# Kernel optimization log

Measured on AMD Instinct MI355X. Metric: run time of the kernel, lower is better.

The kernel has to match this reference:

```python
import jax, jax.numpy as jnp
import numpy as np

D_MODEL, D_K, H = 1024, 64, 16
B, S = 2, 2048

def setup_inputs() -> dict:
    key = jax.random.key(0)
    ks = jax.random.split(key, 9)
    s_in = 1.0 / np.sqrt(D_MODEL)
    x = jax.random.normal(ks[0], (B, S, D_MODEL), dtype=jnp.float32)
    Wq = jax.random.uniform(ks[1], (H, D_MODEL, D_K), jnp.float32, -s_in, s_in)
    bq = jax.random.uniform(ks[2], (H, D_K), jnp.float32, -s_in, s_in)
    Wk = jax.random.uniform(ks[3], (H, D_MODEL, D_K), jnp.float32, -s_in, s_in)
    bk = jax.random.uniform(ks[4], (H, D_K), jnp.float32, -s_in, s_in)
    Wv = jax.random.uniform(ks[5], (H, D_MODEL, D_K), jnp.float32, -s_in, s_in)
    bv = jax.random.uniform(ks[6], (H, D_K), jnp.float32, -s_in, s_in)
    Wo = jax.random.uniform(ks[7], (D_MODEL, D_MODEL), jnp.float32, -s_in, s_in)
    bo = jax.random.uniform(ks[8], (D_MODEL,), jnp.float32, -s_in, s_in)
    return {"x": x, "Wq": Wq, "bq": bq, "Wk": Wk, "bk": bk,
            "Wv": Wv, "bv": bv, "Wo": Wo, "bo": bo}

def reference(x, Wq, bq, Wk, bk, Wv, bv, Wo, bo):
    # PositionLinear = Linear + ReLU (the ReLU is part of the original math)
    Q = jax.nn.relu(jnp.einsum('bsd,hdk->bhsk', x, Wq) + bq[:, None, :])
    K = jax.nn.relu(jnp.einsum('bsd,hdk->bhsk', x, Wk) + bk[:, None, :])
    V = jax.nn.relu(jnp.einsum('bsd,hdk->bhsk', x, Wv) + bv[:, None, :])
    scale = jnp.sqrt(jnp.float32(Q.shape[-1]))
    scores = jnp.einsum('bhsk,bhtk->bhst', Q, K) / scale  # [B,H,S,S]
    attn = jax.nn.softmax(scores, axis=-1)
    ctx = jnp.einsum('bhst,bhtk->bhsk', attn, V)
    # concat heads along feature dim (head order matches torch.cat(output, 2))
    ctx = jnp.transpose(ctx, (0, 2, 1, 3)).reshape(x.shape[0], x.shape[1], -1)
    out = jax.nn.relu(ctx @ Wo + bo)
    return out
```

## Files before the change

### kernel.cpp

```cpp
#include <hip/hip_runtime.h>
#include <cstddef>

#define D_MODEL 1024
#define DK 64
#define NH 16
#define NB 2
#define SEQ 2048

typedef __attribute__((ext_vector_type(8))) short bf16x8;
typedef __attribute__((ext_vector_type(4))) float floatx4;
typedef __attribute__((ext_vector_type(2))) unsigned uintx2;

static __device__ __forceinline__ unsigned short f2bf(float f) {
    union { float f; unsigned u; } v; v.f = f;
    unsigned r = (v.u + 0x7fffu + ((v.u >> 16) & 1u)) >> 16;
    return (unsigned short)r;
}

static __device__ __forceinline__ unsigned pk2bf(float lo, float hi) {
    unsigned ua = __float_as_uint(lo) + 0x8000u;
    unsigned ub = __float_as_uint(hi) + 0x8000u;
    return __builtin_amdgcn_perm(ub, ua, 0x07060302u);
}

static __device__ __forceinline__ float swz16(float x) {
    return __int_as_float(__builtin_amdgcn_ds_swizzle(__float_as_int(x), 0x401F));
}

static __device__ __forceinline__ void gld16(const unsigned short* g, unsigned short* l) {
    __builtin_amdgcn_global_load_lds(
        (const __attribute__((address_space(1))) unsigned int*)g,
        (__attribute__((address_space(3))) unsigned int*)l, 16, 0, 0);
}

__global__ __launch_bounds__(256) void convert_x(const float* __restrict__ x,
                                                 unsigned short* __restrict__ xb)
{
    const size_t i = ((size_t)blockIdx.x * 256 + threadIdx.x) * 16;
#pragma unroll
    for (int c = 0; c < 16; c += 4) {
        float4 v = *(const float4*)&x[i + c];
        uint2 pk;
        pk.x = (unsigned)f2bf(v.x) | ((unsigned)f2bf(v.y) << 16);
        pk.y = (unsigned)f2bf(v.z) | ((unsigned)f2bf(v.w) << 16);
        *(uint2*)&xb[i + c] = pk;
    }
}

__global__ __launch_bounds__(256) void pack_w(
    const float* __restrict__ Wq, const float* __restrict__ Wk,
    const float* __restrict__ Wv, const float* __restrict__ Wo,
    unsigned short* __restrict__ Bqkv, unsigned short* __restrict__ Bo)
{
    __shared__ float T[64][65];
    const int t   = blockIdx.x;
    const int tid = threadIdx.x;
    const int rr   = tid >> 2;
    const int cseg = (tid & 3) * 16;

    const float* src;
    unsigned short* dst;
    if (t < 768) {
        const int proj = t / 256, rem = t % 256;
        const int h = rem >> 4, d0 = (rem & 15) * 64;
        const float* W = proj == 0 ? Wq : (proj == 1 ? Wk : Wv);
        src = W + ((size_t)h * 1024 + d0) * 64;
#pragma unroll
        for (int c = 0; c < 16; c += 4) {
            float4 v = *(const float4*)&src[(size_t)rr * 64 + cseg + c];
            T[rr][cseg + c + 0] = v.x; T[rr][cseg + c + 1] = v.y;
            T[rr][cseg + c + 2] = v.z; T[rr][cseg + c + 3] = v.w;
        }
        __syncthreads();
        dst = &Bqkv[((size_t)proj * 1024 + h * 64 + rr) * 1024 + d0 + cseg];
    } else {
        const int t2 = t - 768;
        const int k0 = (t2 >> 4) * 64, nb0 = (t2 & 15) * 64;
#pragma unroll
        for (int c = 0; c < 16; c += 4) {
            float4 v = *(const float4*)&Wo[(size_t)(k0 + rr) * 1024 + nb0 + cseg + c];
            T[rr][cseg + c + 0] = v.x; T[rr][cseg + c + 1] = v.y;
            T[rr][cseg + c + 2] = v.z; T[rr][cseg + c + 3] = v.w;
        }
        __syncthreads();
        dst = &Bo[(size_t)(nb0 + rr) * 1024 + k0 + cseg];
    }
    unsigned int w[8];
#pragma unroll
    for (int ii = 0; ii < 8; ii++) {
        unsigned short lo = f2bf(T[cseg + ii * 2 + 0][rr]);
        unsigned short hi = f2bf(T[cseg + ii * 2 + 1][rr]);
        w[ii] = (unsigned)lo | ((unsigned)hi << 16);
    }
    *(uint4*)(dst + 0) = make_uint4(w[0], w[1], w[2], w[3]);
    *(uint4*)(dst + 8) = make_uint4(w[4], w[5], w[6], w[7]);
}

__global__ __launch_bounds__(256) void gemm_qkv(
    const unsigned short* __restrict__ Abf,
    const unsigned short* __restrict__ Bp,
    const float* __restrict__ bq, const float* __restrict__ bk,
    const float* __restrict__ bv,
    unsigned short* __restrict__ Qo, unsigned short* __restrict__ Ko,
    unsigned short* __restrict__ Vo)
{
    __shared__ __align__(16) unsigned short As[128 * 32];
    __shared__ __align__(16) unsigned short Bs[128 * 32];

    const int tid  = threadIdx.x;
    const int wv   = tid >> 6, lane = tid & 63;
    const int m0   = blockIdx.x * 128;
    const int n0   = blockIdx.y * 128;
    const int lq   = lane & 15, g = lane >> 4;
    const int wm   = (wv >> 1) * 64;
    const int wn   = (wv & 1) * 64;
    const int srow = lane >> 2;
    const int sseg = (lane & 3) * 8;

    floatx4 acc[4][4];
#pragma unroll
    for (int i = 0; i < 4; i++)
#pragma unroll
        for (int j = 0; j < 4; j++) acc[i][j] = (floatx4){0.f, 0.f, 0.f, 0.f};

    for (int k0 = 0; k0 < 1024; k0 += 32) {
#pragma unroll
        for (int r = 0; r < 2; r++) {
            const int chunk = wv * 2 + r;
            const int row   = chunk * 16 + srow;
            gld16(&Abf[(size_t)(m0 + row) * 1024 + k0 + sseg], &As[chunk * 512]);
            gld16(&Bp [(size_t)(n0 + row) * 1024 + k0 + sseg], &Bs[chunk * 512]);
        }
        __syncthreads();
        bf16x8 af[4], bfv[4];
#pragma unroll
        for (int i = 0; i < 4; i++)
            af[i] = *(const bf16x8*)&As[(wm + i * 16 + lq) * 32 + g * 8];
#pragma unroll
        for (int j = 0; j < 4; j++)
            bfv[j] = *(const bf16x8*)&Bs[(wn + j * 16 + lq) * 32 + g * 8];
#pragma unroll
        for (int i = 0; i < 4; i++)
#pragma unroll
            for (int j = 0; j < 4; j++)
                acc[i][j] = __builtin_amdgcn_mfma_f32_16x16x32_bf16(af[i], bfv[j], acc[i][j], 0, 0, 0);
        __syncthreads();
    }

    const int proj = n0 >> 10;
    const float* bias = proj == 0 ? bq : (proj == 1 ? bk : bv);
    unsigned short* OutQK = proj == 0 ? Qo : Ko;

#pragma unroll
    for (int j = 0; j < 4; j++) {
        const int n  = n0 + wn + j * 16 + lq;
        const int nn = n & 1023;
        const int h  = nn >> 6, dk = nn & 63;
        const float bb = bias[nn];
#pragma unroll
        for (int i = 0; i < 4; i++) {
            const int mbase = m0 + wm + i * 16 + g * 4;
            const int b_ = mbase >> 11;
            const int s_ = mbase & (SEQ - 1);
            const int bh = b_ * NH + h;
            if (proj < 2) {
                const size_t fb = (((size_t)bh * 128 + (s_ >> 4)) * 2 + (dk >> 5)) * 512
                                + (size_t)((((dk & 31) >> 3) * 16) + (s_ & 15)) * 8 + (dk & 7);
#pragma unroll
                for (int r = 0; r < 4; r++)
                    OutQK[fb + (size_t)r * 8] = f2bf(fmaxf(acc[i][j][r] + bb, 0.f));
            } else {
                const size_t fb = ((((size_t)bh * 32 + (s_ >> 6)) * 4 + (dk >> 4)) * 2
                                   + ((s_ >> 5) & 1)) * 512
                                + (size_t)((((s_ & 31) >> 3) * 16) + (dk & 15)) * 8 + (s_ & 7);
                uint2 pk;
                pk.x = (unsigned)f2bf(fmaxf(acc[i][j][0] + bb, 0.f))
                     | ((unsigned)f2bf(fmaxf(acc[i][j][1] + bb, 0.f)) << 16);
                pk.y = (unsigned)f2bf(fmaxf(acc[i][j][2] + bb, 0.f))
                     | ((unsigned)f2bf(fmaxf(acc[i][j][3] + bb, 0.f)) << 16);
                *(uint2*)&Vo[fb] = pk;
            }
        }
    }
}

__global__ __launch_bounds__(512, 4) void attn_kernel(
    const unsigned short* __restrict__ Qf,
    const unsigned short* __restrict__ Kf,
    const unsigned short* __restrict__ Vf,
    unsigned short* __restrict__ ctxb)
{
    __shared__ __align__(16) unsigned short KVs[2][16384];
    __shared__ float Lx[4][2][64];

    const int blk = blockIdx.x;
    const int xcd = blk & 7;
    const int j_  = blk >> 3;
    const int bh  = xcd * 4 + (j_ & 3);
    const int qt  = j_ >> 2;

    const int tid  = threadIdx.x;
    const int wv   = tid >> 6;
    const int lane = tid & 63;
    const int lq   = lane & 15;
    const int g    = lane >> 4;
    const int qq   = wv >> 1;
    const int kh   = wv & 1;

    const int q0 = qt * 128 + qq * 32;

    bf16x8 qa[2], qb[2];
    const size_t qfB = ((size_t)bh * 128 + (q0 >> 4)) * 1024 + (size_t)lane * 8;
#pragma unroll
    for (int t = 0; t < 2; t++) {
        qa[t] = *(const bf16x8*)&Qf[qfB + (size_t)t * 1024];
        qb[t] = *(const bf16x8*)&Qf[qfB + (size_t)t * 1024 + 512];
    }

    const float C  = 0.18033688011112042f;
    const float MC = 2.8853900817779267f;

    const unsigned short* KtB = &Kf[(size_t)bh * 131072];
    const unsigned short* VtB = &Vf[(size_t)bh * 131072];

    float l[2] = {0.f, 0.f};
    floatx4 acc[2][4];
#pragma unroll
    for (int t = 0; t < 2; t++)
#pragma unroll
        for (int n = 0; n < 4; n++) acc[t][n] = (floatx4){0.f, 0.f, 0.f, 0.f};

#pragma unroll
    for (int r = 0; r < 2; r++) {
        const int c = wv * 2 + r;
        gld16(&KtB[(size_t)c * 512 + lane * 8], &KVs[0][c * 512]);
        gld16(&VtB[(size_t)c * 512 + lane * 8], &KVs[0][8192 + c * 512]);
    }
    __syncthreads();

    for (int jt = 0; jt < SEQ / 128; jt++) {
        const int buf = jt & 1;

        const int jn = (jt + 1) & (SEQ / 128 - 1);
        const unsigned short* ktn = &KtB[(size_t)jn * 8192];
        const unsigned short* vtn = &VtB[(size_t)jn * 8192];
#pragma unroll
        for (int r = 0; r < 2; r++) {
            const int c = wv * 2 + r;
            gld16(&ktn[(size_t)c * 512 + lane * 8], &KVs[buf ^ 1][c * 512]);
            gld16(&vtn[(size_t)c * 512 + lane * 8], &KVs[buf ^ 1][8192 + c * 512]);
        }

        const unsigned short* kb = &KVs[buf][0];
        const unsigned short* vb = &KVs[buf][8192];

#pragma unroll
        for (int s = 0; s < 2; s++) {
            const int kg = 4 * kh + 2 * s;
            bf16x8 a0 = *(const bf16x8*)&kb[(kg + 0) * 1024 + lane * 8];
            bf16x8 a1 = *(const bf16x8*)&kb[(kg + 0) * 1024 + 512 + lane * 8];
            bf16x8 a2 = *(const bf16x8*)&kb[(kg + 1) * 1024 + lane * 8];
            bf16x8 a3 = *(const bf16x8*)&kb[(kg + 1) * 1024 + 512 + lane * 8];
            bf16x8 vr[4];
#pragma unroll
            for (int n = 0; n < 4; n++)
                vr[n] = *(const bf16x8*)&vb[(kh * 4 + n) * 1024 + s * 512 + lane * 8];

#pragma unroll
            for (int t = 0; t < 2; t++) {
                floatx4 s0 = (floatx4){0.f, 0.f, 0.f, 0.f};
                floatx4 s1 = (floatx4){0.f, 0.f, 0.f, 0.f};
                __builtin_amdgcn_s_setprio(1);
                s0 = __builtin_amdgcn_mfma_f32_16x16x32_bf16(a0, qa[t], s0, 0, 0, 0);
                s0 = __builtin_amdgcn_mfma_f32_16x16x32_bf16(a1, qb[t], s0, 0, 0, 0);
                s1 = __builtin_amdgcn_mfma_f32_16x16x32_bf16(a2, qa[t], s1, 0, 0, 0);
                s1 = __builtin_amdgcn_mfma_f32_16x16x32_bf16(a3, qb[t], s1, 0, 0, 0);
                __builtin_amdgcn_s_setprio(0);

                float p00 = __builtin_amdgcn_exp2f(fmaf(s0[0], C, -MC));
                float p01 = __builtin_amdgcn_exp2f(fmaf(s0[1], C, -MC));
                float p02 = __builtin_amdgcn_exp2f(fmaf(s0[2], C, -MC));
                float p03 = __builtin_amdgcn_exp2f(fmaf(s0[3], C, -MC));
                l[t] += (p00 + p01) + (p02 + p03);
                unsigned d0 = pk2bf(p00, p01);
                unsigned d1 = pk2bf(p02, p03);

                float p10 = __builtin_amdgcn_exp2f(fmaf(s1[0], C, -MC));
                float p11 = __builtin_amdgcn_exp2f(fmaf(s1[1], C, -MC));
                float p12 = __builtin_amdgcn_exp2f(fmaf(s1[2], C, -MC));
                float p13 = __builtin_amdgcn_exp2f(fmaf(s1[3], C, -MC));
                l[t] += (p10 + p11) + (p12 + p13);
                unsigned d2 = pk2bf(p10, p11);
                unsigned d3 = pk2bf(p12, p13);

                uintx2 r02 = __builtin_amdgcn_permlane32_swap(d0, d2, false, false);
                uintx2 r13 = __builtin_amdgcn_permlane32_swap(d1, d3, false, false);
                uintx2 f02 = __builtin_amdgcn_permlane16_swap(r02.x, r02.y, false, false);
                uintx2 f13 = __builtin_amdgcn_permlane16_swap(r13.x, r13.y, false, false);

                union { unsigned u[4]; bf16x8 v; } pbu;
                pbu.u[0] = f02.x;
                pbu.u[1] = f13.x;
                pbu.u[2] = f02.y;
                pbu.u[3] = f13.y;

                __builtin_amdgcn_s_setprio(1);
#pragma unroll
                for (int n = 0; n < 4; n++)
                    acc[t][n] = __builtin_amdgcn_mfma_f32_16x16x32_bf16(vr[n], pbu.v, acc[t][n], 0, 0, 0);
                __builtin_amdgcn_s_setprio(0);
            }
        }

        __syncthreads();
    }

#pragma unroll
    for (int t = 0; t < 2; t++) {
        l[t] += swz16(l[t]);
        l[t] += __shfl_xor(l[t], 32, 64);
    }

    float* red = (float*)&KVs[0][0] + (size_t)qq * 2048;
    if (kh == 1) {
#pragma unroll
        for (int t = 0; t < 2; t++) {
            Lx[qq][t][lane] = l[t];
#pragma unroll
            for (int n = 0; n < 4; n++)
                *(floatx4*)&red[(t * 4 + n) * 256 + lane * 4] = acc[t][n];
        }
    }
    __syncthreads();
    if (kh == 0) {
        const int b_ = bh >> 4, h_ = bh & 15;
#pragma unroll
        for (int t = 0; t < 2; t++) {
            const float lt = l[t] + Lx[qq][t][lane];
            const float li = 1.f / lt;
#pragma unroll
            for (int n = 0; n < 4; n++) {
                floatx4 a = acc[t][n];
                floatx4 b = *(const floatx4*)&red[(t * 4 + n) * 256 + lane * 4];
                uint2 pk;
                pk.x = pk2bf((a[0] + b[0]) * li, (a[1] + b[1]) * li);
                pk.y = pk2bf((a[2] + b[2]) * li, (a[3] + b[3]) * li);
                *(uint2*)&ctxb[((size_t)(b_ * SEQ) + q0 + t * 16 + lq) * D_MODEL
                               + h_ * DK + n * 16 + g * 4] = pk;
            }
        }
    }
}

__global__ __launch_bounds__(256) void gemm_o(
    const unsigned short* __restrict__ Abf,
    const unsigned short* __restrict__ Bp,
    const float* __restrict__ bo,
    float* __restrict__ out)
{
    __shared__ __align__(16) unsigned short As[64 * 32];
    __shared__ __align__(16) unsigned short Bs[64 * 32];

    const int tid  = threadIdx.x;
    const int wv   = tid >> 6, lane = tid & 63;
    const int bid  = blockIdx.x;
    const int swz  = (bid & 7) * 128 + (bid >> 3);
    const int m0   = (swz & 63) * 64;
    const int n0   = (swz >> 6) * 64;
    const int lq   = lane & 15, g = lane >> 4;
    const int wm   = (wv >> 1) * 32;
    const int wn   = (wv & 1) * 32;
    const int srow = lane >> 2;
    const int sseg = (lane & 3) * 8;

    floatx4 acc[2][2];
#pragma unroll
    for (int i = 0; i < 2; i++)
#pragma unroll
        for (int j = 0; j < 2; j++) acc[i][j] = (floatx4){0.f, 0.f, 0.f, 0.f};

    for (int k0 = 0; k0 < 1024; k0 += 32) {
        const int row = wv * 16 + srow;
        gld16(&Abf[(size_t)(m0 + row) * 1024 + k0 + sseg], &As[wv * 512]);
        gld16(&Bp [(size_t)(n0 + row) * 1024 + k0 + sseg], &Bs[wv * 512]);
        __syncthreads();
        bf16x8 af[2], bfv[2];
#pragma unroll
        for (int i = 0; i < 2; i++)
            af[i] = *(const bf16x8*)&As[(wm + i * 16 + lq) * 32 + g * 8];
#pragma unroll
        for (int j = 0; j < 2; j++)
            bfv[j] = *(const bf16x8*)&Bs[(wn + j * 16 + lq) * 32 + g * 8];
#pragma unroll
        for (int i = 0; i < 2; i++)
#pragma unroll
            for (int j = 0; j < 2; j++)
                acc[i][j] = __builtin_amdgcn_mfma_f32_16x16x32_bf16(af[i], bfv[j], acc[i][j], 0, 0, 0);
        __syncthreads();
    }

#pragma unroll
    for (int j = 0; j < 2; j++) {
        const int n  = n0 + wn + j * 16 + lq;
        const float bb = bo[n];
#pragma unroll
        for (int i = 0; i < 2; i++) {
#pragma unroll
            for (int r = 0; r < 4; r++) {
                const int m = m0 + wm + i * 16 + g * 4 + r;
                out[(size_t)m * 1024 + n] = fmaxf(acc[i][j][r] + bb, 0.f);
            }
        }
    }
}

extern "C" void kernel_launch(void* const* d_in, const int* in_sizes, int n_in,
                              void* d_out, int out_size, void* d_ws, size_t ws_size,
                              hipStream_t stream) {
    const float* x  = (const float*)d_in[0];
    const float* Wq = (const float*)d_in[1];
    const float* bq = (const float*)d_in[2];
    const float* Wk = (const float*)d_in[3];
    const float* bk = (const float*)d_in[4];
    const float* Wv = (const float*)d_in[5];
    const float* bv = (const float*)d_in[6];
    const float* Wo = (const float*)d_in[7];
    const float* bo = (const float*)d_in[8];
    float* out = (float*)d_out;

    const size_t perE = (size_t)NB * NH * SEQ * DK;
    unsigned short* xbf  = (unsigned short*)d_ws;
    unsigned short* Bqkv = xbf  + (size_t)4096 * 1024;
    unsigned short* Bo   = Bqkv + (size_t)3072 * 1024;
    unsigned short* Qfr  = Bo   + (size_t)1024 * 1024;
    unsigned short* Kfr  = Qfr + perE;
    unsigned short* Vfr  = Kfr + perE;
    unsigned short* Cbf  = Vfr + perE;

    convert_x<<<1024, 256, 0, stream>>>(x, xbf);
    pack_w<<<1024, 256, 0, stream>>>(Wq, Wk, Wv, Wo, Bqkv, Bo);
    gemm_qkv<<<dim3(32, 24), 256, 0, stream>>>(xbf, Bqkv, bq, bk, bv, Qfr, Kfr, Vfr);
    attn_kernel<<<512, 512, 0, stream>>>(Qfr, Kfr, Vfr, Cbf);
    gemm_o<<<1024, 256, 0, stream>>>(Cbf, Bo, bo, out);
}
```

Before: 193.2 us.

## Read K/V fragments directly from global memory in attention and merge prep kernels

The attention kernel drops its double-buffered LDS staging of K/V tiles (global_load_lds plus a per-iteration barrier). Each wave now loads its K and V fragments straight from global memory, relying on cache reuse across the waves of a block. It also removes the s_setprio hints around the MFMAs and unrolls the key loop by two. The x conversion and weight packing kernels are merged into one launch to save a kernel launch. The risk is redundant global/L2 traffic, because each K/V tile is now read by several waves instead of once into shared memory.

```diff
diff --git a/kernel.cpp b/kernel.cpp
--- a/kernel.cpp
+++ b/kernel.cpp
@@ -33,28 +33,29 @@
         (__attribute__((address_space(3))) unsigned int*)l, 16, 0, 0);
 }
 
-__global__ __launch_bounds__(256) void convert_x(const float* __restrict__ x,
-                                                 unsigned short* __restrict__ xb)
-{
-    const size_t i = ((size_t)blockIdx.x * 256 + threadIdx.x) * 16;
-#pragma unroll
-    for (int c = 0; c < 16; c += 4) {
-        float4 v = *(const float4*)&x[i + c];
-        uint2 pk;
-        pk.x = (unsigned)f2bf(v.x) | ((unsigned)f2bf(v.y) << 16);
-        pk.y = (unsigned)f2bf(v.z) | ((unsigned)f2bf(v.w) << 16);
-        *(uint2*)&xb[i + c] = pk;
-    }
-}
-
-__global__ __launch_bounds__(256) void pack_w(
+__global__ __launch_bounds__(256) void prep(
+    const float* __restrict__ x, unsigned short* __restrict__ xb,
     const float* __restrict__ Wq, const float* __restrict__ Wk,
     const float* __restrict__ Wv, const float* __restrict__ Wo,
     unsigned short* __restrict__ Bqkv, unsigned short* __restrict__ Bo)
 {
     __shared__ float T[64][65];
-    const int t   = blockIdx.x;
     const int tid = threadIdx.x;
+
+    if (blockIdx.x < 1024) {
+        const size_t i = ((size_t)blockIdx.x * 256 + tid) * 16;
+#pragma unroll
+        for (int c = 0; c < 16; c += 4) {
+            float4 v = *(const float4*)&x[i + c];
+            uint2 pk;
+            pk.x = (unsigned)f2bf(v.x) | ((unsigned)f2bf(v.y) << 16);
+            pk.y = (unsigned)f2bf(v.z) | ((unsigned)f2bf(v.w) << 16);
+            *(uint2*)&xb[i + c] = pk;
+        }
+        return;
+    }
+
+    const int t   = blockIdx.x - 1024;
     const int rr   = tid >> 2;
     const int cseg = (tid & 3) * 16;
 
@@ -190,7 +191,7 @@
     const unsigned short* __restrict__ Vf,
     unsigned short* __restrict__ ctxb)
 {
-    __shared__ __align__(16) unsigned short KVs[2][16384];
+    __shared__ float red[4][2048];
     __shared__ float Lx[4][2][64];
 
     const int blk = blockIdx.x;
@@ -230,29 +231,10 @@
 #pragma unroll
         for (int n = 0; n < 4; n++) acc[t][n] = (floatx4){0.f, 0.f, 0.f, 0.f};
 
-#pragma unroll
-    for (int r = 0; r < 2; r++) {
-        const int c = wv * 2 + r;
-        gld16(&KtB[(size_t)c * 512 + lane * 8], &KVs[0][c * 512]);
-        gld16(&VtB[(size_t)c * 512 + lane * 8], &KVs[0][8192 + c * 512]);
-    }
-    __syncthreads();
-
+#pragma unroll 2
     for (int jt = 0; jt < SEQ / 128; jt++) {
-        const int buf = jt & 1;
-
-        const int jn = (jt + 1) & (SEQ / 128 - 1);
-        const unsigned short* ktn = &KtB[(size_t)jn * 8192];
-        const unsigned short* vtn = &VtB[(size_t)jn * 8192];
-#pragma unroll
-        for (int r = 0; r < 2; r++) {
-            const int c = wv * 2 + r;
-            gld16(&ktn[(size_t)c * 512 + lane * 8], &KVs[buf ^ 1][c * 512]);
-            gld16(&vtn[(size_t)c * 512 + lane * 8], &KVs[buf ^ 1][8192 + c * 512]);
-        }
-
-        const unsigned short* kb = &KVs[buf][0];
-        const unsigned short* vb = &KVs[buf][8192];
+        const unsigned short* kb = KtB + (size_t)jt * 8192;
+        const unsigned short* vb = VtB + (size_t)jt * 8192;
 
 #pragma unroll
         for (int s = 0; s < 2; s++) {
@@ -270,12 +252,10 @@
             for (int t = 0; t < 2; t++) {
                 floatx4 s0 = (floatx4){0.f, 0.f, 0.f, 0.f};
                 floatx4 s1 = (floatx4){0.f, 0.f, 0.f, 0.f};
-                __builtin_amdgcn_s_setprio(1);
                 s0 = __builtin_amdgcn_mfma_f32_16x16x32_bf16(a0, qa[t], s0, 0, 0, 0);
                 s0 = __builtin_amdgcn_mfma_f32_16x16x32_bf16(a1, qb[t], s0, 0, 0, 0);
                 s1 = __builtin_amdgcn_mfma_f32_16x16x32_bf16(a2, qa[t], s1, 0, 0, 0);
                 s1 = __builtin_amdgcn_mfma_f32_16x16x32_bf16(a3, qb[t], s1, 0, 0, 0);
-                __builtin_amdgcn_s_setprio(0);
 
                 float p00 = __builtin_amdgcn_exp2f(fmaf(s0[0], C, -MC));
                 float p01 = __builtin_amdgcn_exp2f(fmaf(s0[1], C, -MC));
@@ -304,15 +284,11 @@
                 pbu.u[2] = f02.y;
                 pbu.u[3] = f13.y;
 
-                __builtin_amdgcn_s_setprio(1);
 #pragma unroll
                 for (int n = 0; n < 4; n++)
                     acc[t][n] = __builtin_amdgcn_mfma_f32_16x16x32_bf16(vr[n], pbu.v, acc[t][n], 0, 0, 0);
-                __builtin_amdgcn_s_setprio(0);
             }
         }
-
-        __syncthreads();
     }
 
 #pragma unroll
@@ -321,14 +297,13 @@
         l[t] += __shfl_xor(l[t], 32, 64);
     }
 
-    float* red = (float*)&KVs[0][0] + (size_t)qq * 2048;
     if (kh == 1) {
 #pragma unroll
         for (int t = 0; t < 2; t++) {
             Lx[qq][t][lane] = l[t];
 #pragma unroll
             for (int n = 0; n < 4; n++)
-                *(floatx4*)&red[(t * 4 + n) * 256 + lane * 4] = acc[t][n];
+                *(floatx4*)&red[qq][(t * 4 + n) * 256 + lane * 4] = acc[t][n];
         }
     }
     __syncthreads();
@@ -341,7 +316,7 @@
 #pragma unroll
             for (int n = 0; n < 4; n++) {
                 floatx4 a = acc[t][n];
-                floatx4 b = *(const floatx4*)&red[(t * 4 + n) * 256 + lane * 4];
+                floatx4 b = *(const floatx4*)&red[qq][(t * 4 + n) * 256 + lane * 4];
                 uint2 pk;
                 pk.x = pk2bf((a[0] + b[0]) * li, (a[1] + b[1]) * li);
                 pk.y = pk2bf((a[2] + b[2]) * li, (a[3] + b[3]) * li);
@@ -437,8 +412,7 @@
     unsigned short* Vfr  = Kfr + perE;
     unsigned short* Cbf  = Vfr + perE;
 
-    convert_x<<<1024, 256, 0, stream>>>(x, xbf);
-    pack_w<<<1024, 256, 0, stream>>>(Wq, Wk, Wv, Wo, Bqkv, Bo);
+    prep<<<2048, 256, 0, stream>>>(x, xbf, Wq, Wk, Wv, Wo, Bqkv, Bo);
     gemm_qkv<<<dim3(32, 24), 256, 0, stream>>>(xbf, Bqkv, bq, bk, bv, Qfr, Kfr, Vfr);
     attn_kernel<<<512, 512, 0, stream>>>(Qfr, Kfr, Vfr, Cbf);
     gemm_o<<<1024, 256, 0, stream>>>(Cbf, Bo, bo, out);
```

Measured after the change: 192.5 us. Within noise of the previous version (-0.4%).
